# Kernel tuning notes

Hardware: AMD Instinct MI355X
Metric: run time of the kernel (lower is better)

Reference implementation:

```python
import jax, jax.numpy as jnp
import numpy as np

B, N, F = 64, 512, 30          # batch, pf candidates, raw features
NDIM0, NDIM = 2, 4             # coord dims: layer0 uses 2, rest use n_dim_gnn=4
NOUT, NLAYERS = 64, 5          # GNN layer width / count
NDENSE = 128
BN_EPS = 1e-3                  # keras BatchNormalization default epsilon


def setup_inputs() -> dict:
    key = jax.random.key(0)
    ks = jax.random.split(key, 20)
    xx = jax.random.normal(ks[0], (B, N, F), jnp.float32)
    # validity mask: first L_b candidates valid
    lengths = jax.random.randint(ks[1], (B,), N // 4, N + 1)
    valid = (jnp.arange(N)[None, :] < lengths[:, None]).astype(jnp.float32)
    pt = jax.random.randint(ks[2], (B, N), 0, 8).astype(jnp.float32)
    pvq = jax.random.randint(ks[3], (B, N), 0, 8).astype(jnp.float32)
    fpv = jax.random.randint(ks[4], (B, N), 0, 4).astype(jnp.float32)
    xx = xx.at[:, :, 0].set(valid).at[:, :, 27].set(pt).at[:, :, 28].set(pvq).at[:, :, 29].set(fpv)
    g = lambda k, s, sc=0.05: jax.random.normal(k, s, jnp.float32) * sc
    d_in0 = 33  # 2+2+2 embeddings + 27 float features
    return {
        "xx": xx,
        "emb1": g(ks[5], (8, 2), 0.5),
        "emb2": g(ks[6], (8, 2), 0.5),
        "emb3": g(ks[7], (4, 2), 0.5),
        "A0": g(ks[8], ((d_in0 + 1) * 2 - 1, NOUT)),   # [67,64]
        "b0": g(ks[9], (NOUT,)),
        "A_rest": g(ks[10], (NLAYERS - 1, (NOUT + 1) * 2 - 1, NOUT)),  # [4,129,64]
        "b_rest": g(ks[11], (NLAYERS - 1, NOUT)),
        "bn_gamma": jnp.ones((NLAYERS, NOUT), jnp.float32),
        "bn_beta": jnp.zeros((NLAYERS, NOUT), jnp.float32),
        "dW0": g(ks[12], (N * NOUT, NDENSE), 0.01),
        "db0": g(ks[13], (NDENSE,)),
        "dW1": g(ks[14], (NDENSE, NDENSE)),
        "db1": g(ks[15], (NDENSE,)),
        "dbn_gamma": jnp.ones((2, NDENSE), jnp.float32),
        "dbn_beta": jnp.zeros((2, NDENSE), jnp.float32),
        "W2": g(ks[16], (NDENSE, 2)),
        "b2": g(ks[17], (2,)),
    }


def _bn(x, g, b):
    # inference BatchNorm with moving_mean=0, moving_var=1 (initial stats)
    return g * x * (1.0 / jnp.sqrt(1.0 + BN_EPS)) + b


def _gnn_layer(x, mask, n_dim, A, b):
    # x: [B,N,Fin], mask: [B,N]. Original builds [B,N,N,Fin+1] via tile/reshape;
    # algebraically the reduction over senders i factorizes:
    #   ss_feat[b,j] = x[b,j] * mask[b,j] * sum_i exp(-10*d_ij)
    #   ss_last[b,j] = mask[b,j] * sum_i d_ij * exp(-10*d_ij)
    c = x[..., -n_dim:]
    diff = c[:, :, None, :] - c[:, None, :, :]      # [B,N,N,n_dim]
    dist = jnp.sum(diff * diff, axis=-1)            # [B,N,N] squared distance
    w = jnp.exp(-10.0 * dist)
    S = jnp.sum(w, axis=1)                          # [B,N] per receiver j
    T = jnp.sum(dist * w, axis=1)                   # [B,N]
    ss_feat = x * (mask * S)[..., None] - x         # subtract concat(x, 0)
    ss_last = (mask * T)[..., None]
    xcat = jnp.concatenate([x, ss_feat, ss_last], axis=-1)  # [B,N,2*Fin+1]
    return (xcat @ A + b) * mask[..., None]


def _forward(xx, emb1, emb2, emb3, A0, b0, A_rest, b_rest, bn_gamma, bn_beta,
             dW0, db0, dW1, db1, dbn_gamma, dbn_beta, W2, b2):
    mask = xx[:, :, 0]
    e1 = emb1[jnp.abs(xx[:, :, 27]).astype(jnp.int32)]
    e2 = emb2[jnp.abs(xx[:, :, 28]).astype(jnp.int32)]
    e3 = emb3[jnp.abs(xx[:, :, 29]).astype(jnp.int32)]
    x = jnp.concatenate([e1, e2, e3, xx[:, :, :27]], axis=-1)  # [B,N,33]
    x = jnp.tanh(_bn(_gnn_layer(x, mask, NDIM0, A0, b0), bn_gamma[0], bn_beta[0]))
    for k in range(NLAYERS - 1):
        x = _gnn_layer(x, mask, NDIM, A_rest[k], b_rest[k])
        x = jnp.tanh(_bn(x, bn_gamma[k + 1], bn_beta[k + 1]))
    x = x.reshape(B, N * NOUT)
    x = jax.nn.sigmoid(_bn(x @ dW0 + db0, dbn_gamma[0], dbn_beta[0]))
    x = jax.nn.sigmoid(_bn(x @ dW1 + db1, dbn_gamma[1], dbn_beta[1]))
    x = x @ W2 + b2                                  # [B,2]
    # mode == 'dm': concat zeros on the right
    return jnp.concatenate([x, jnp.zeros((B, 2), x.dtype)], axis=1)


def reference(xx, emb1, emb2, emb3, A0, b0, A_rest, b_rest, bn_gamma, bn_beta,
              dW0, db0, dW1, db1, dbn_gamma, dbn_beta, W2, b2):
    return _forward(xx, emb1, emb2, emb3, A0, b0, A_rest, b_rest, bn_gamma, bn_beta,
                    dW0, db0, dW1, db1, dbn_gamma, dbn_beta, W2, b2)
```

## Files before the change

### kernel.cpp

```cpp
#include <hip/hip_runtime.h>
#include <math.h>

#define B_ 64
#define N_ 512
#define R_ (B_*N_)
#define INV_S 0.9995003746877732f

__device__ __forceinline__ float fast_tanh(float y){
  return 1.f - 2.f*__builtin_amdgcn_rcpf(1.f + __expf(2.f*y));
}
__device__ __forceinline__ float fast_sigmoid(float v){
  return __builtin_amdgcn_rcpf(1.f + __expf(-v));
}

template<int L0>
__global__ __launch_bounds__(256, 4) void gnn_layer(
    const float* __restrict__ xx, const float* __restrict__ xin,
    const float4* __restrict__ cin, const float* __restrict__ A,
    const float* __restrict__ bias, const float* __restrict__ gamma,
    const float* __restrict__ beta,
    const float* __restrict__ emb1, const float* __restrict__ emb2,
    const float* __restrict__ emb3,
    const float* __restrict__ maskb,
    float* __restrict__ maskout,
    float4* __restrict__ cout,
    float* __restrict__ xout)
{
  constexpr int KP = L0 ? 36 : 64;
  constexpr int K  = L0 ? 33 : 64;
  __shared__ float4 cl[512];
  __shared__ float alo[KP*64];
  __shared__ float ahi[KP*64];
  __shared__ float xl[L0 ? 64*36 : 4];
  __shared__ float spart[256], tpart[256];
  __shared__ float scl[64], tcl[64], ml[64];

  int tid = threadIdx.x;
  int jc = blockIdx.x;
  int b  = blockIdx.y;
  int rbase = b*N_, jloc = jc*64;

  if constexpr (L0){
    for (int i = tid; i < 512; i += 256){
      const float* row = xx + (size_t)(rbase+i)*30;
      cl[i] = make_float4(row[25], row[26], 0.f, 0.f);
    }
  } else {
    for (int i = tid; i < 512; i += 256)
      cl[i] = cin[rbase + i];
  }

  if constexpr (L0){
    for (int idx = tid; idx < KP*64; idx += 256){
      int f = idx >> 6;
      alo[idx] = (f < K) ? A[idx] : 0.f;
      ahi[idx] = (f < K) ? A[(size_t)K*64 + idx] : 0.f;
    }
  } else {
    const float4* A4 = (const float4*)A;
    float4* alo4 = (float4*)alo;
    float4* ahi4 = (float4*)ahi;
    for (int idx = tid; idx < 1024; idx += 256){
      alo4[idx] = A4[idx];
      ahi4[idx] = A4[1024 + idx];
    }
  }

  if constexpr (L0){
    if (tid < 64){
      int r = rbase + jloc + tid;
      const float* row = xx + (size_t)r*30;
      float v[30];
#pragma unroll
      for (int i=0;i<30;i++) v[i] = row[i];
      int i1 = (int)fabsf(v[27]);
      int i2 = (int)fabsf(v[28]);
      int i3 = (int)fabsf(v[29]);
      float* o = &xl[tid*36];
      o[0]=emb1[i1*2+0]; o[1]=emb1[i1*2+1];
      o[2]=emb2[i2*2+0]; o[3]=emb2[i2*2+1];
      o[4]=emb3[i3*2+0]; o[5]=emb3[i3*2+1];
#pragma unroll
      for (int i=0;i<27;i++) o[6+i] = v[i];
      o[33]=0.f; o[34]=0.f; o[35]=0.f;
      ml[tid] = v[0];
      maskout[r] = v[0];
    }
  } else {
    if (tid < 64) ml[tid] = maskb[rbase + jloc + tid];
  }
  __syncthreads();

  {
    int jj = tid & 63, q = tid >> 6;
    float4 cj = cl[jloc + jj];
    float Ss = 0.f, Ts = 0.f;
    int base = q*128;
#pragma unroll 8
    for (int i=0;i<128;i++){
      float4 ci = cl[base+i];
      float d0 = cj.x-ci.x, d1 = cj.y-ci.y, d2 = cj.z-ci.z, d3 = cj.w-ci.w;
      float dist = d0*d0 + d1*d1 + d2*d2 + d3*d3;
      float w = __expf(-10.f*dist);
      Ss += w;
      Ts += dist*w;
    }
    spart[tid] = Ss;
    tpart[tid] = Ts;
  }
  __syncthreads();
  if (tid < 64){
    float S = spart[tid] + spart[tid+64] + spart[tid+128] + spart[tid+192];
    float T = tpart[tid] + tpart[tid+64] + tpart[tid+128] + tpart[tid+192];
    float m = ml[tid];
    scl[tid] = m*S - 1.f;
    tcl[tid] = m*T;
  }
  __syncthreads();

  int o0 = (tid & 15)*4, r0 = (tid >> 4)*4;
  const float* xb = xin + (size_t)(rbase + jloc + r0)*64;
  float4 acc1[4], acc2[4];
#pragma unroll
  for (int rr=0;rr<4;rr++){
    acc1[rr] = make_float4(0.f,0.f,0.f,0.f);
    acc2[rr] = make_float4(0.f,0.f,0.f,0.f);
  }
#pragma unroll 2
  for (int kc = 0; kc < KP; kc += 4){
    float4 a1[4], a2[4], xv[4];
#pragma unroll
    for (int uu=0;uu<4;uu++){
      a1[uu] = *(const float4*)&alo[(kc+uu)*64 + o0];
      a2[uu] = *(const float4*)&ahi[(kc+uu)*64 + o0];
    }
#pragma unroll
    for (int rr=0;rr<4;rr++){
      if constexpr (L0) xv[rr] = *(const float4*)&xl[(r0+rr)*36 + kc];
      else              xv[rr] = *(const float4*)&xb[rr*64 + kc];
    }
#pragma unroll
    for (int uu=0;uu<4;uu++){
#pragma unroll
      for (int rr=0;rr<4;rr++){
        float xu = ((const float*)&xv[rr])[uu];
        acc1[rr].x = fmaf(xu, a1[uu].x, acc1[rr].x);
        acc1[rr].y = fmaf(xu, a1[uu].y, acc1[rr].y);
        acc1[rr].z = fmaf(xu, a1[uu].z, acc1[rr].z);
        acc1[rr].w = fmaf(xu, a1[uu].w, acc1[rr].w);
        acc2[rr].x = fmaf(xu, a2[uu].x, acc2[rr].x);
        acc2[rr].y = fmaf(xu, a2[uu].y, acc2[rr].y);
        acc2[rr].z = fmaf(xu, a2[uu].z, acc2[rr].z);
        acc2[rr].w = fmaf(xu, a2[uu].w, acc2[rr].w);
      }
    }
  }

  float4 alast = *(const float4*)&A[(size_t)2*K*64 + o0];
  float4 bo = *(const float4*)&bias[o0];
  float4 go = *(const float4*)&gamma[o0];
  float4 be = *(const float4*)&beta[o0];
#pragma unroll
  for (int rr=0;rr<4;rr++){
    int r = rbase + jloc + r0 + rr;
    float sc = scl[r0+rr], tc = tcl[r0+rr], m = ml[r0+rr];
    float4 v;
    v.x = (acc1[rr].x + sc*acc2[rr].x + tc*alast.x + bo.x)*m;
    v.y = (acc1[rr].y + sc*acc2[rr].y + tc*alast.y + bo.y)*m;
    v.z = (acc1[rr].z + sc*acc2[rr].z + tc*alast.z + bo.z)*m;
    v.w = (acc1[rr].w + sc*acc2[rr].w + tc*alast.w + bo.w)*m;
    float4 t;
    t.x = fast_tanh(go.x*(v.x*INV_S) + be.x);
    t.y = fast_tanh(go.y*(v.y*INV_S) + be.y);
    t.z = fast_tanh(go.z*(v.z*INV_S) + be.z);
    t.w = fast_tanh(go.w*(v.w*INV_S) + be.w);
    *(float4*)&xout[(size_t)r*64 + o0] = t;
    if (cout && o0 == 60) cout[r] = t;
  }
}

__global__ __launch_bounds__(256) void dense0_partial(
    const float* __restrict__ X, const float* __restrict__ W,
    float* __restrict__ partial)
{
  __shared__ float xt[64*32];
  __shared__ float wt[32*128];
  int tid = threadIdx.x;
  int k0 = blockIdx.x*128;
  int og = (tid & 15)*8;
  int rg = (tid >> 4)*4;
  float acc[4][8];
#pragma unroll
  for (int a=0;a<4;a++)
#pragma unroll
    for (int u=0;u<8;u++) acc[a][u]=0.f;
  for (int kt = 0; kt < 128; kt += 32){
    __syncthreads();
    for (int idx = tid; idx < 512; idx += 256){
      int r = idx >> 3, kq = idx & 7;
      *(float4*)&xt[r*32 + kq*4] =
          *(const float4*)&X[(size_t)r*32768 + k0 + kt + kq*4];
    }
    {
      const float4* Wc = (const float4*)&W[(size_t)(k0+kt)*128];
      float4* wt4 = (float4*)wt;
      for (int idx = tid; idx < 1024; idx += 256) wt4[idx] = Wc[idx];
    }
    __syncthreads();
#pragma unroll 4
    for (int k=0;k<32;k++){
      float4 w0 = *(const float4*)&wt[k*128 + og];
      float4 w1 = *(const float4*)&wt[k*128 + og + 4];
      float xs[4];
#pragma unroll
      for (int rr=0;rr<4;rr++) xs[rr] = xt[(rg+rr)*32 + k];
#pragma unroll
      for (int rr=0;rr<4;rr++){
        acc[rr][0] = fmaf(xs[rr], w0.x, acc[rr][0]);
        acc[rr][1] = fmaf(xs[rr], w0.y, acc[rr][1]);
        acc[rr][2] = fmaf(xs[rr], w0.z, acc[rr][2]);
        acc[rr][3] = fmaf(xs[rr], w0.w, acc[rr][3]);
        acc[rr][4] = fmaf(xs[rr], w1.x, acc[rr][4]);
        acc[rr][5] = fmaf(xs[rr], w1.y, acc[rr][5]);
        acc[rr][6] = fmaf(xs[rr], w1.z, acc[rr][6]);
        acc[rr][7] = fmaf(xs[rr], w1.w, acc[rr][7]);
      }
    }
  }
  float* pb = partial + (size_t)blockIdx.x*8192;
#pragma unroll
  for (int rr=0;rr<4;rr++){
    *(float4*)&pb[(rg+rr)*128 + og]     = *(float4*)&acc[rr][0];
    *(float4*)&pb[(rg+rr)*128 + og + 4] = *(float4*)&acc[rr][4];
  }
}

__global__ __launch_bounds__(256) void dense_head(
    const float* __restrict__ partial,
    const float* __restrict__ db0, const float* __restrict__ dg0,
    const float* __restrict__ dbb0,
    const float* __restrict__ dW1, const float* __restrict__ db1,
    const float* __restrict__ dg1, const float* __restrict__ dbb1,
    const float* __restrict__ W2, const float* __restrict__ b2,
    float* __restrict__ out)
{
  __shared__ float sred[256];
  __shared__ float h[128];
  __shared__ float red0[128], red1[128];
  int tid = threadIdx.x;
  int b = blockIdx.x;
  int o = tid & 127, ph = tid >> 7;
  float s = 0.f;
#pragma unroll 16
  for (int p = ph*128; p < ph*128+128; p++)
    s += partial[(size_t)p*8192 + b*128 + o];
  sred[tid] = s;
  __syncthreads();
  if (tid < 128){
    float sum = sred[tid] + sred[tid+128];
    float v = dg0[tid]*((sum + db0[tid])*INV_S) + dbb0[tid];
    h[tid] = fast_sigmoid(v);
  }
  __syncthreads();
  if (tid < 128){
    float acc = 0.f;
#pragma unroll 8
    for (int k=0;k<128;k++) acc = fmaf(h[k], dW1[k*128 + tid], acc);
    float v = dg1[tid]*((acc + db1[tid])*INV_S) + dbb1[tid];
    float h1 = fast_sigmoid(v);
    red0[tid] = h1 * W2[tid*2+0];
    red1[tid] = h1 * W2[tid*2+1];
  }
  __syncthreads();
  for (int st=64; st>0; st>>=1){
    if (tid < st){ red0[tid] += red0[tid+st]; red1[tid] += red1[tid+st]; }
    __syncthreads();
  }
  if (tid == 0){
    out[b*4+0] = red0[0] + b2[0];
    out[b*4+1] = red1[0] + b2[1];
    out[b*4+2] = 0.f;
    out[b*4+3] = 0.f;
  }
}

extern "C" void kernel_launch(void* const* d_in, const int* in_sizes, int n_in,
                              void* d_out, int out_size, void* d_ws, size_t ws_size,
                              hipStream_t stream)
{
  const float* xx   = (const float*)d_in[0];
  const float* emb1 = (const float*)d_in[1];
  const float* emb2 = (const float*)d_in[2];
  const float* emb3 = (const float*)d_in[3];
  const float* A0   = (const float*)d_in[4];
  const float* b0   = (const float*)d_in[5];
  const float* Ar   = (const float*)d_in[6];
  const float* br   = (const float*)d_in[7];
  const float* bng  = (const float*)d_in[8];
  const float* bnb  = (const float*)d_in[9];
  const float* dW0  = (const float*)d_in[10];
  const float* db0  = (const float*)d_in[11];
  const float* dW1  = (const float*)d_in[12];
  const float* db1  = (const float*)d_in[13];
  const float* dbg  = (const float*)d_in[14];
  const float* dbb  = (const float*)d_in[15];
  const float* W2   = (const float*)d_in[16];
  const float* b2   = (const float*)d_in[17];

  float* ws = (float*)d_ws;
  float* xA      = ws;
  float* xB      = xA + (size_t)R_*64;
  float* partial = xB + (size_t)R_*64;
  float* maskb   = partial + (size_t)256*8192;
  float4* cbuf   = (float4*)(maskb + R_);

  dim3 lgrid(8, 64);
  gnn_layer<1><<<lgrid, 256, 0, stream>>>(
      xx, nullptr, nullptr, A0, b0, bng, bnb, emb1, emb2, emb3,
      nullptr, maskb, cbuf, xA);
  float* bufs[2] = {xA, xB};
  int curi = 0;
  for (int k=0;k<4;k++){
    const float* cur = bufs[curi];
    float* nxt = bufs[1-curi];
    gnn_layer<0><<<lgrid, 256, 0, stream>>>(
        xx, cur, cbuf, Ar + (size_t)k*129*64, br + k*64,
        bng + (k+1)*64, bnb + (k+1)*64, emb1, emb2, emb3,
        maskb, nullptr, (k < 3) ? cbuf : nullptr, nxt);
    curi ^= 1;
  }
  const float* x5 = bufs[curi];

  dense0_partial<<<256, 256, 0, stream>>>(x5, dW0, partial);
  dense_head<<<B_, 256, 0, stream>>>(partial, db0, dbg, dbb,
                                     dW1, db1, dbg + 128, dbb + 128,
                                     W2, b2, (float*)d_out);
}
```

Measured before the change: 219.4 us.

## Double GNN block threads, read coordinates from global, ping-pong coordinate buffers

```diff
diff --git a/kernel.cpp b/kernel.cpp
--- a/kernel.cpp
+++ b/kernel.cpp
@@ -14,7 +14,7 @@
 }
 
 template<int L0>
-__global__ __launch_bounds__(256, 4) void gnn_layer(
+__global__ __launch_bounds__(512, 4) void gnn_layer(
     const float* __restrict__ xx, const float* __restrict__ xin,
     const float4* __restrict__ cin, const float* __restrict__ A,
     const float* __restrict__ bias, const float* __restrict__ gamma,
@@ -28,11 +28,10 @@
 {
   constexpr int KP = L0 ? 36 : 64;
   constexpr int K  = L0 ? 33 : 64;
-  __shared__ float4 cl[512];
   __shared__ float alo[KP*64];
   __shared__ float ahi[KP*64];
   __shared__ float xl[L0 ? 64*36 : 4];
-  __shared__ float spart[256], tpart[256];
+  __shared__ float spart[512], tpart[512];
   __shared__ float scl[64], tcl[64], ml[64];
 
   int tid = threadIdx.x;
@@ -41,17 +40,7 @@
   int rbase = b*N_, jloc = jc*64;
 
   if constexpr (L0){
-    for (int i = tid; i < 512; i += 256){
-      const float* row = xx + (size_t)(rbase+i)*30;
-      cl[i] = make_float4(row[25], row[26], 0.f, 0.f);
-    }
-  } else {
-    for (int i = tid; i < 512; i += 256)
-      cl[i] = cin[rbase + i];
-  }
-
-  if constexpr (L0){
-    for (int idx = tid; idx < KP*64; idx += 256){
+    for (int idx = tid; idx < KP*64; idx += 512){
       int f = idx >> 6;
       alo[idx] = (f < K) ? A[idx] : 0.f;
       ahi[idx] = (f < K) ? A[(size_t)K*64 + idx] : 0.f;
@@ -60,7 +49,7 @@
     const float4* A4 = (const float4*)A;
     float4* alo4 = (float4*)alo;
     float4* ahi4 = (float4*)ahi;
-    for (int idx = tid; idx < 1024; idx += 256){
+    for (int idx = tid; idx < 1024; idx += 512){
       alo4[idx] = A4[idx];
       ahi4[idx] = A4[1024 + idx];
     }
@@ -89,60 +78,81 @@
   } else {
     if (tid < 64) ml[tid] = maskb[rbase + jloc + tid];
   }
-  __syncthreads();
 
   {
-    int jj = tid & 63, q = tid >> 6;
-    float4 cj = cl[jloc + jj];
+    int jj = tid & 63, ic = tid >> 6;
     float Ss = 0.f, Ts = 0.f;
-    int base = q*128;
+    if constexpr (L0){
+      const float* xb = xx + (size_t)rbase*30;
+      float cjx = xb[(jloc+jj)*30 + 25];
+      float cjy = xb[(jloc+jj)*30 + 26];
+      int base = ic*64;
 #pragma unroll 8
-    for (int i=0;i<128;i++){
-      float4 ci = cl[base+i];
-      float d0 = cj.x-ci.x, d1 = cj.y-ci.y, d2 = cj.z-ci.z, d3 = cj.w-ci.w;
-      float dist = d0*d0 + d1*d1 + d2*d2 + d3*d3;
-      float w = __expf(-10.f*dist);
-      Ss += w;
-      Ts += dist*w;
+      for (int i=0;i<64;i++){
+        float cix = xb[(base+i)*30 + 25];
+        float ciy = xb[(base+i)*30 + 26];
+        float d0 = cjx-cix, d1 = cjy-ciy;
+        float dist = d0*d0 + d1*d1;
+        float w = __expf(-10.f*dist);
+        Ss += w; Ts += dist*w;
+      }
+    } else {
+      const float4* cb = cin + rbase;
+      float4 cj = cb[jloc + jj];
+      int base = ic*64;
+#pragma unroll 8
+      for (int i=0;i<64;i++){
+        float4 ci = cb[base+i];
+        float d0 = cj.x-ci.x, d1 = cj.y-ci.y, d2 = cj.z-ci.z, d3 = cj.w-ci.w;
+        float dist = d0*d0 + d1*d1 + d2*d2 + d3*d3;
+        float w = __expf(-10.f*dist);
+        Ss += w; Ts += dist*w;
+      }
     }
     spart[tid] = Ss;
     tpart[tid] = Ts;
   }
   __syncthreads();
+
   if (tid < 64){
-    float S = spart[tid] + spart[tid+64] + spart[tid+128] + spart[tid+192];
-    float T = tpart[tid] + tpart[tid+64] + tpart[tid+128] + tpart[tid+192];
+    float S = 0.f, T = 0.f;
+#pragma unroll
+    for (int c=0;c<8;c++){
+      S += spart[tid + 64*c];
+      T += tpart[tid + 64*c];
+    }
     float m = ml[tid];
     scl[tid] = m*S - 1.f;
     tcl[tid] = m*T;
   }
   __syncthreads();
 
-  int o0 = (tid & 15)*4, r0 = (tid >> 4)*4;
-  const float* xb = xin + (size_t)(rbase + jloc + r0)*64;
-  float4 acc1[4], acc2[4];
-#pragma unroll
-  for (int rr=0;rr<4;rr++){
+  int cg = tid & 15, rg = tid >> 4;
+  int o0 = cg*4, lr0 = rg*2;
+  const float* xb2 = xin + (size_t)(rbase + jloc)*64;
+  float4 acc1[2], acc2[2];
+#pragma unroll
+  for (int rr=0;rr<2;rr++){
     acc1[rr] = make_float4(0.f,0.f,0.f,0.f);
     acc2[rr] = make_float4(0.f,0.f,0.f,0.f);
   }
 #pragma unroll 2
   for (int kc = 0; kc < KP; kc += 4){
-    float4 a1[4], a2[4], xv[4];
+    float4 a1[4], a2[4], xv[2];
 #pragma unroll
     for (int uu=0;uu<4;uu++){
       a1[uu] = *(const float4*)&alo[(kc+uu)*64 + o0];
       a2[uu] = *(const float4*)&ahi[(kc+uu)*64 + o0];
     }
 #pragma unroll
-    for (int rr=0;rr<4;rr++){
-      if constexpr (L0) xv[rr] = *(const float4*)&xl[(r0+rr)*36 + kc];
-      else              xv[rr] = *(const float4*)&xb[rr*64 + kc];
+    for (int rr=0;rr<2;rr++){
+      if constexpr (L0) xv[rr] = *(const float4*)&xl[(lr0+rr)*36 + kc];
+      else              xv[rr] = *(const float4*)&xb2[(lr0+rr)*64 + kc];
     }
 #pragma unroll
     for (int uu=0;uu<4;uu++){
 #pragma unroll
-      for (int rr=0;rr<4;rr++){
+      for (int rr=0;rr<2;rr++){
         float xu = ((const float*)&xv[rr])[uu];
         acc1[rr].x = fmaf(xu, a1[uu].x, acc1[rr].x);
         acc1[rr].y = fmaf(xu, a1[uu].y, acc1[rr].y);
@@ -161,9 +171,10 @@
   float4 go = *(const float4*)&gamma[o0];
   float4 be = *(const float4*)&beta[o0];
 #pragma unroll
-  for (int rr=0;rr<4;rr++){
-    int r = rbase + jloc + r0 + rr;
-    float sc = scl[r0+rr], tc = tcl[r0+rr], m = ml[r0+rr];
+  for (int rr=0;rr<2;rr++){
+    int lr = lr0 + rr;
+    int r = rbase + jloc + lr;
+    float sc = scl[lr], tc = tcl[lr], m = ml[lr];
     float4 v;
     v.x = (acc1[rr].x + sc*acc2[rr].x + tc*alast.x + bo.x)*m;
     v.y = (acc1[rr].y + sc*acc2[rr].y + tc*alast.y + bo.y)*m;
@@ -175,7 +186,7 @@
     t.z = fast_tanh(go.z*(v.z*INV_S) + be.z);
     t.w = fast_tanh(go.w*(v.w*INV_S) + be.w);
     *(float4*)&xout[(size_t)r*64 + o0] = t;
-    if (cout && o0 == 60) cout[r] = t;
+    if (cout && cg == 15) cout[r] = t;
   }
 }
 
@@ -308,30 +319,31 @@
   const float* b2   = (const float*)d_in[17];
 
   float* ws = (float*)d_ws;
-  float* xA      = ws;
-  float* xB      = xA + (size_t)R_*64;
-  float* partial = xB + (size_t)R_*64;
-  float* maskb   = partial + (size_t)256*8192;
-  float4* cbuf   = (float4*)(maskb + R_);
+  float*  xA      = ws;
+  float*  xB      = xA + (size_t)R_*64;
+  float*  partial = xB + (size_t)R_*64;
+  float*  maskb   = partial + (size_t)256*8192;
+  float4* cb0     = (float4*)(maskb + R_);
+  float4* cb1     = cb0 + R_;
 
   dim3 lgrid(8, 64);
-  gnn_layer<1><<<lgrid, 256, 0, stream>>>(
+  gnn_layer<1><<<lgrid, 512, 0, stream>>>(
       xx, nullptr, nullptr, A0, b0, bng, bnb, emb1, emb2, emb3,
-      nullptr, maskb, cbuf, xA);
-  float* bufs[2] = {xA, xB};
-  int curi = 0;
-  for (int k=0;k<4;k++){
-    const float* cur = bufs[curi];
-    float* nxt = bufs[1-curi];
-    gnn_layer<0><<<lgrid, 256, 0, stream>>>(
-        xx, cur, cbuf, Ar + (size_t)k*129*64, br + k*64,
-        bng + (k+1)*64, bnb + (k+1)*64, emb1, emb2, emb3,
-        maskb, nullptr, (k < 3) ? cbuf : nullptr, nxt);
-    curi ^= 1;
-  }
-  const float* x5 = bufs[curi];
-
-  dense0_partial<<<256, 256, 0, stream>>>(x5, dW0, partial);
+      nullptr, maskb, cb1, xA);
+  gnn_layer<0><<<lgrid, 512, 0, stream>>>(
+      xx, xA, cb1, Ar + (size_t)0*129*64, br + 0*64, bng + 64, bnb + 64,
+      emb1, emb2, emb3, maskb, nullptr, cb0, xB);
+  gnn_layer<0><<<lgrid, 512, 0, stream>>>(
+      xx, xB, cb0, Ar + (size_t)1*129*64, br + 1*64, bng + 128, bnb + 128,
+      emb1, emb2, emb3, maskb, nullptr, cb1, xA);
+  gnn_layer<0><<<lgrid, 512, 0, stream>>>(
+      xx, xA, cb1, Ar + (size_t)2*129*64, br + 2*64, bng + 192, bnb + 192,
+      emb1, emb2, emb3, maskb, nullptr, cb0, xB);
+  gnn_layer<0><<<lgrid, 512, 0, stream>>>(
+      xx, xB, cb0, Ar + (size_t)3*129*64, br + 3*64, bng + 256, bnb + 256,
+      emb1, emb2, emb3, maskb, nullptr, nullptr, xA);
+
+  dense0_partial<<<256, 256, 0, stream>>>(xA, dW0, partial);
   dense_head<<<B_, 256, 0, stream>>>(partial, db0, dbg, dbb,
                                      dW1, db1, dbg + 128, dbb + 128,
                                      W2, b2, (float*)d_out);
```

New measurement: 216.7 us. No clear change (-1.2%).
